# Kernel tuning notes

Measured on AMD Instinct MI355X. Metric: run time of the kernel, lower is better.

## Reference

```python
import jax, jax.numpy as jnp
import numpy as np

N = 50000
D = 128
T = 1024
K = 10
GAMMA = 1.0
CHUNK = 64  # anchors processed per step to avoid a [T,N,D] intermediate


def setup_inputs() -> dict:
    key = jax.random.key(0)
    k1, k2, k3, k4 = jax.random.split(key, 4)
    return {
        "out1": jax.random.normal(k1, (N, D), dtype=jnp.float32),
        "out2": jax.random.normal(k2, (N, D), dtype=jnp.float32),
        "anchor1_org": jax.random.randint(k3, (T,), 0, N, dtype=jnp.int64 if jax.config.jax_enable_x64 else jnp.int32),
        "anchor2_org": jax.random.randint(k4, (T,), 0, N, dtype=jnp.int64 if jax.config.jax_enable_x64 else jnp.int32),
    }


def _mine_neg(anchor_vecs, G):
    # anchor_vecs: [T, D], G: [N, D] -> indices of K nearest (L1) rows of G, [T*K]
    a = anchor_vecs.reshape(T // CHUNK, CHUNK, D)

    def body(chunk):
        # L1 distances [CHUNK, N]
        dist = jnp.sum(jnp.abs(chunk[:, None, :] - G[None, :, :]), axis=-1)
        _, idx = jax.lax.top_k(-dist, K)  # k smallest distances
        return idx

    idx = jax.lax.map(body, a)  # [T//CHUNK, CHUNK, K]
    return idx.reshape(T * K)


def reference(out1, out2, anchor1_org, anchor2_org):
    # negative mining (mirrors cdist + argsort[:k] on detached arrays)
    neg1 = _mine_neg(out1[anchor1_org], out2)  # negatives in graph 2 for anchor1
    neg2 = _mine_neg(out2[anchor2_org], out1)  # negatives in graph 1 for anchor2

    anchor1 = jnp.repeat(anchor1_org, K)  # [T*K]
    anchor2 = jnp.repeat(anchor2_org, K)

    a1 = out1[anchor1]
    a2 = out2[anchor2]
    n1 = out2[neg1]
    n2 = out1[neg2]

    A = jnp.sum(jnp.abs(a1 - a2), axis=1)
    Dm = A + GAMMA
    L1 = jnp.sum(jax.nn.relu(Dm - jnp.sum(jnp.abs(a1 - n1), axis=1)))
    L2 = jnp.sum(jax.nn.relu(Dm - jnp.sum(jnp.abs(a2 - n2), axis=1)))
    return (L1 + L2) / (T * K)
```

## Files before the change

### kernel.cpp

```cpp
#include <hip/hip_runtime.h>
#include <stdint.h>


#define NROWS 50000
#define DDIM  128
#define TT    1024
#define KK    10
#define NCH   64
#define CH    782
#define TILES 16
#define TT2   (2 * TT)
#define TROWS 16

typedef float f32x2 __attribute__((ext_vector_type(2)));
typedef float f32x4 __attribute__((ext_vector_type(4)));

__device__ __forceinline__ void topk_insert(float (&val)[KK], int (&idx)[KK],
                                            float cv, int ci) {
#pragma unroll
  for (int i = 0; i < KK; i++) {
    const bool lt = cv < val[i];
    const float tv = lt ? val[i] : cv;
    const int ti = lt ? idx[i] : ci;
    val[i] = lt ? cv : val[i];
    idx[i] = lt ? ci : idx[i];
    cv = tv;
    ci = ti;
  }
}

__global__ __launch_bounds__(64, 2) void mine_kernel(
    const float* __restrict__ out1, const float* __restrict__ out2,
    const int* __restrict__ anc1, const int* __restrict__ anc2,
    float* __restrict__ cand_val, int* __restrict__ cand_idx) {
  const int lane = threadIdx.x;
  const int bid = blockIdx.x;
  const int chunk = ((bid >> 8) << 3) | (bid & 7);
  const int combo = (bid >> 3) & 31;
  const int dir = combo >> 4;
  const int tile = combo & 15;

  const float* __restrict__ A = dir ? out2 : out1;
  const float* __restrict__ G = dir ? out1 : out2;
  const int* __restrict__ anc = dir ? anc2 : anc1;

  const int a = tile * 64 + lane;
  const int arow = anc[a];

  f32x2 av[DDIM / 2];
  {
    const f32x4* ap = (const f32x4*)(A + (size_t)arow * DDIM);
#pragma unroll
    for (int j = 0; j < DDIM / 4; j++) {
      const f32x4 v = ap[j];
      av[2 * j] = (f32x2){v.x, v.y};
      av[2 * j + 1] = (f32x2){v.z, v.w};
    }
  }

  float val[KK];
  int idx[KK];
#pragma unroll
  for (int i = 0; i < KK; i++) {
    val[i] = 3.4e38f;
    idx[i] = 0;
  }

  const int r0 = chunk * CH;
  const int r1 = (r0 + CH < NROWS) ? (r0 + CH) : NROWS;
  const int nt = (r1 - r0 + TROWS - 1) / TROWS;

  __shared__ float gt[2][TROWS * DDIM];

  auto STAGE = [&](int b, int rs) {
    const float* gsrc = G + (size_t)rs * DDIM + lane * 4;
    float* ldst = &gt[b][0];
#pragma unroll
    for (int c = 0; c < (TROWS * DDIM) / 256; c++) {
      __builtin_amdgcn_global_load_lds(
          (const __attribute__((address_space(1))) uint32_t*)(gsrc + c * 256),
          (__attribute__((address_space(3))) uint32_t*)(ldst + c * 256),
          16, 0, 0);
    }
  };

  auto RS = [&](int ts) { return ts > NROWS - TROWS ? NROWS - TROWS : ts; };

  STAGE(0, RS(r0));
  asm volatile("s_waitcnt vmcnt(0)" ::: "memory");

  int buf = 0;
  for (int t = 0; t < nt; t++) {
    const int ts = r0 + t * TROWS;
    const int rs = RS(ts);
    if (t + 1 < nt) STAGE(buf ^ 1, RS(ts + TROWS));

    const int rend = (ts + TROWS < r1) ? ts + TROWS : r1;
    for (int r = ts; r < rend; r++) {
      const f32x4* lp = (const f32x4*)&gt[buf][(r - rs) * DDIM];
      float c0 = 0.f, c1 = 0.f, c2 = 0.f, c3 = 0.f;
#pragma unroll
      for (int j = 0; j < DDIM / 4; j++) {
        const f32x4 g = lp[j];
        const f32x2 d0 = av[2 * j] - (f32x2){g.x, g.y};
        const f32x2 d1 = av[2 * j + 1] - (f32x2){g.z, g.w};
        c0 += fabsf(d0.x);
        c1 += fabsf(d0.y);
        c2 += fabsf(d1.x);
        c3 += fabsf(d1.y);
      }
      const float acc = (c0 + c1) + (c2 + c3);
      if (acc < val[KK - 1]) topk_insert(val, idx, acc, r);
    }
    asm volatile("s_waitcnt vmcnt(0)" ::: "memory");
    buf ^= 1;
  }

  const int slot = dir * TT + a;
#pragma unroll
  for (int i = 0; i < KK; i++) {
    const size_t o = (size_t)(chunk * KK + i) * TT2 + slot;
    cand_val[o] = val[i];
    cand_idx[o] = idx[i];
  }
}

__global__ void merge_kernel(const float* __restrict__ cand_val,
                             const int* __restrict__ cand_idx,
                             int* __restrict__ neg) {
  const int tid = blockIdx.x * blockDim.x + threadIdx.x;
  if (tid >= TT2) return;
  float val[KK];
  int idx[KK];
#pragma unroll
  for (int i = 0; i < KK; i++) {
    val[i] = 3.4e38f;
    idx[i] = 0;
  }
  for (int c = 0; c < NCH * KK; c++) {
    const float v = cand_val[(size_t)c * TT2 + tid];
    if (v < val[KK - 1]) topk_insert(val, idx, v, cand_idx[(size_t)c * TT2 + tid]);
  }
#pragma unroll
  for (int i = 0; i < KK; i++) neg[(size_t)tid * KK + i] = idx[i];
}

__global__ void zero_kernel(float* __restrict__ out) {
  if (threadIdx.x == 0) out[0] = 0.f;
}

__global__ void loss_kernel(const float* __restrict__ out1,
                            const float* __restrict__ out2,
                            const int* __restrict__ anc1,
                            const int* __restrict__ anc2,
                            const int* __restrict__ neg,
                            float* __restrict__ out) {
  const int lane = threadIdx.x & 63;
  const int w = threadIdx.x >> 6;
  const int t = blockIdx.x * 4 + w;
  const int a1 = anc1[t];
  const int a2 = anc2[t];
  const int e = lane * 2;

  const f32x2 x1 = *(const f32x2*)(out1 + (size_t)a1 * DDIM + e);
  const f32x2 x2 = *(const f32x2*)(out2 + (size_t)a2 * DDIM + e);

  float ap = fabsf(x1.x - x2.x) + fabsf(x1.y - x2.y);
#pragma unroll
  for (int o = 32; o > 0; o >>= 1) ap += __shfl_xor(ap, o, 64);
  const float Dm = ap + 1.0f;

  float s = 0.f;
  for (int k = 0; k < KK; k++) {
    const int n1 = neg[(size_t)t * KK + k];
    const int n2 = neg[(size_t)(TT + t) * KK + k];
    const f32x2 v1 = *(const f32x2*)(out2 + (size_t)n1 * DDIM + e);
    const f32x2 v2 = *(const f32x2*)(out1 + (size_t)n2 * DDIM + e);
    float d1 = fabsf(x1.x - v1.x) + fabsf(x1.y - v1.y);
    float d2 = fabsf(x2.x - v2.x) + fabsf(x2.y - v2.y);
#pragma unroll
    for (int o = 32; o > 0; o >>= 1) {
      d1 += __shfl_xor(d1, o, 64);
      d2 += __shfl_xor(d2, o, 64);
    }
    s += fmaxf(Dm - d1, 0.f) + fmaxf(Dm - d2, 0.f);
  }
  if (lane == 0) atomicAdd(out, s * (1.0f / (TT * KK)));
}

extern "C" void kernel_launch(void* const* d_in, const int* in_sizes, int n_in,
                              void* d_out, int out_size, void* d_ws,
                              size_t ws_size, hipStream_t stream) {
  const float* out1 = (const float*)d_in[0];
  const float* out2 = (const float*)d_in[1];
  const int* anc1 = (const int*)d_in[2];
  const int* anc2 = (const int*)d_in[3];

  float* cand_val = (float*)d_ws;
  int* cand_idx = (int*)(cand_val + (size_t)NCH * KK * TT2);
  int* neg = cand_idx + (size_t)NCH * KK * TT2;
  float* out = (float*)d_out;

  hipLaunchKernelGGL(mine_kernel, dim3(2 * TILES * NCH), dim3(64), 0, stream,
                     out1, out2, anc1, anc2, cand_val, cand_idx);
  hipLaunchKernelGGL(merge_kernel, dim3(8), dim3(256), 0, stream, cand_val,
                     cand_idx, neg);
  hipLaunchKernelGGL(zero_kernel, dim3(1), dim3(64), 0, stream, out);
  hipLaunchKernelGGL(loss_kernel, dim3(TT / 4), dim3(256), 0, stream, out1,
                     out2, anc1, anc2, neg, out);
}
```

Measured before the change: 1.386 ms.

## Split anchor dims across lane pairs, widen mine blocks, two-level top-k merge

Each anchor's 128-dim L1 distance is now split across two lanes that each hold half the vector and combine partial sums with a shuffle. This halves per-thread register use for the anchor and doubles thread parallelism. Mining blocks grow to 256 threads (128 anchors) sharing each staged LDS tile, with __syncthreads replacing per-wave waits. The serial 640-candidate merge is split into a parallel 8-way partial merge followed by a small final merge. The costs are a duplicated top-k insertion in both lanes of each pair and an extra kernel launch.

New measurement: 3.900 ms. +181.4%, slower.

```diff
diff --git a/kernel.cpp b/kernel.cpp
--- a/kernel.cpp
+++ b/kernel.cpp
@@ -8,7 +8,6 @@
 #define KK    10
 #define NCH   64
 #define CH    782
-#define TILES 16
 #define TT2   (2 * TT)
 #define TROWS 16
 
@@ -29,29 +28,32 @@
   }
 }
 
-__global__ __launch_bounds__(64, 2) void mine_kernel(
+__global__ __launch_bounds__(256, 4) void mine_kernel(
     const float* __restrict__ out1, const float* __restrict__ out2,
     const int* __restrict__ anc1, const int* __restrict__ anc2,
     float* __restrict__ cand_val, int* __restrict__ cand_idx) {
-  const int lane = threadIdx.x;
+  const int tid = threadIdx.x;
+  const int lane = tid & 63;
+  const int w = tid >> 6;
   const int bid = blockIdx.x;
-  const int chunk = ((bid >> 8) << 3) | (bid & 7);
-  const int combo = (bid >> 3) & 31;
-  const int dir = combo >> 4;
-  const int tile = combo & 15;
+  const int chunk = ((bid >> 7) << 3) | (bid & 7);
+  const int combo = (bid >> 3) & 15;
+  const int dir = combo >> 3;
+  const int tile = combo & 7;
 
   const float* __restrict__ A = dir ? out2 : out1;
   const float* __restrict__ G = dir ? out1 : out2;
   const int* __restrict__ anc = dir ? anc2 : anc1;
 
-  const int a = tile * 64 + lane;
+  const int half = lane & 1;
+  const int a = tile * 128 + w * 32 + (lane >> 1);
   const int arow = anc[a];
 
-  f32x2 av[DDIM / 2];
+  f32x2 av[DDIM / 4];
   {
-    const f32x4* ap = (const f32x4*)(A + (size_t)arow * DDIM);
-#pragma unroll
-    for (int j = 0; j < DDIM / 4; j++) {
+    const f32x4* ap = (const f32x4*)(A + (size_t)arow * DDIM + half * 64);
+#pragma unroll
+    for (int j = 0; j < 16; j++) {
       const f32x4 v = ap[j];
       av[2 * j] = (f32x2){v.x, v.y};
       av[2 * j + 1] = (f32x2){v.z, v.w};
@@ -73,21 +75,20 @@
   __shared__ float gt[2][TROWS * DDIM];
 
   auto STAGE = [&](int b, int rs) {
-    const float* gsrc = G + (size_t)rs * DDIM + lane * 4;
-    float* ldst = &gt[b][0];
-#pragma unroll
-    for (int c = 0; c < (TROWS * DDIM) / 256; c++) {
+    const float* src = G + (size_t)rs * DDIM + w * 256 + lane * 4;
+    float* dst = &gt[b][w * 256];
+#pragma unroll
+    for (int c = 0; c < 2; c++) {
       __builtin_amdgcn_global_load_lds(
-          (const __attribute__((address_space(1))) uint32_t*)(gsrc + c * 256),
-          (__attribute__((address_space(3))) uint32_t*)(ldst + c * 256),
+          (const __attribute__((address_space(1))) uint32_t*)(src + c * 1024),
+          (__attribute__((address_space(3))) uint32_t*)(dst + c * 1024),
           16, 0, 0);
     }
   };
-
   auto RS = [&](int ts) { return ts > NROWS - TROWS ? NROWS - TROWS : ts; };
 
   STAGE(0, RS(r0));
-  asm volatile("s_waitcnt vmcnt(0)" ::: "memory");
+  __syncthreads();
 
   int buf = 0;
   for (int t = 0; t < nt; t++) {
@@ -97,10 +98,10 @@
 
     const int rend = (ts + TROWS < r1) ? ts + TROWS : r1;
     for (int r = ts; r < rend; r++) {
-      const f32x4* lp = (const f32x4*)&gt[buf][(r - rs) * DDIM];
+      const f32x4* lp = (const f32x4*)&gt[buf][(r - rs) * DDIM + half * 64];
       float c0 = 0.f, c1 = 0.f, c2 = 0.f, c3 = 0.f;
 #pragma unroll
-      for (int j = 0; j < DDIM / 4; j++) {
+      for (int j = 0; j < 16; j++) {
         const f32x4 g = lp[j];
         const f32x2 d0 = av[2 * j] - (f32x2){g.x, g.y};
         const f32x2 d1 = av[2 * j + 1] - (f32x2){g.z, g.w};
@@ -109,27 +110,55 @@
         c2 += fabsf(d1.x);
         c3 += fabsf(d1.y);
       }
-      const float acc = (c0 + c1) + (c2 + c3);
+      const float p = (c0 + c1) + (c2 + c3);
+      const float acc = p + __shfl_xor(p, 1, 64);
       if (acc < val[KK - 1]) topk_insert(val, idx, acc, r);
     }
-    asm volatile("s_waitcnt vmcnt(0)" ::: "memory");
+    __syncthreads();
     buf ^= 1;
   }
 
-  const int slot = dir * TT + a;
-#pragma unroll
-  for (int i = 0; i < KK; i++) {
-    const size_t o = (size_t)(chunk * KK + i) * TT2 + slot;
+  if ((lane & 1) == 0) {
+    const int slot = dir * TT + a;
+#pragma unroll
+    for (int i = 0; i < KK; i++) {
+      const size_t o = (size_t)(chunk * KK + i) * TT2 + slot;
+      cand_val[o] = val[i];
+      cand_idx[o] = idx[i];
+    }
+  }
+}
+
+__global__ void merge1_kernel(float* __restrict__ cand_val,
+                              int* __restrict__ cand_idx) {
+  const int tid = blockIdx.x * blockDim.x + threadIdx.x;
+  const int slot = tid & (TT2 - 1);
+  const int part = tid >> 11;
+  float val[KK];
+  int idx[KK];
+#pragma unroll
+  for (int i = 0; i < KK; i++) {
+    val[i] = 3.4e38f;
+    idx[i] = 0;
+  }
+  for (int q = 0; q < 8 * KK; q++) {
+    const size_t o = (size_t)(part * 8 * KK + q) * TT2 + slot;
+    const float v = cand_val[o];
+    if (v < val[KK - 1]) topk_insert(val, idx, v, cand_idx[o]);
+  }
+#pragma unroll
+  for (int i = 0; i < KK; i++) {
+    const size_t o = (size_t)(part * 8 * KK + i) * TT2 + slot;
     cand_val[o] = val[i];
     cand_idx[o] = idx[i];
   }
 }
 
-__global__ void merge_kernel(const float* __restrict__ cand_val,
-                             const int* __restrict__ cand_idx,
-                             int* __restrict__ neg) {
-  const int tid = blockIdx.x * blockDim.x + threadIdx.x;
-  if (tid >= TT2) return;
+__global__ void merge2_kernel(const float* __restrict__ cand_val,
+                              const int* __restrict__ cand_idx,
+                              int* __restrict__ neg) {
+  const int slot = blockIdx.x * blockDim.x + threadIdx.x;
+  if (slot >= TT2) return;
   float val[KK];
   int idx[KK];
 #pragma unroll
@@ -137,12 +166,14 @@
     val[i] = 3.4e38f;
     idx[i] = 0;
   }
-  for (int c = 0; c < NCH * KK; c++) {
-    const float v = cand_val[(size_t)c * TT2 + tid];
-    if (v < val[KK - 1]) topk_insert(val, idx, v, cand_idx[(size_t)c * TT2 + tid]);
-  }
-#pragma unroll
-  for (int i = 0; i < KK; i++) neg[(size_t)tid * KK + i] = idx[i];
+  for (int part = 0; part < 8; part++)
+    for (int i = 0; i < KK; i++) {
+      const size_t o = (size_t)(part * 8 * KK + i) * TT2 + slot;
+      const float v = cand_val[o];
+      if (v < val[KK - 1]) topk_insert(val, idx, v, cand_idx[o]);
+    }
+#pragma unroll
+  for (int i = 0; i < KK; i++) neg[(size_t)slot * KK + i] = idx[i];
 }
 
 __global__ void zero_kernel(float* __restrict__ out) {
@@ -201,9 +232,11 @@
   int* neg = cand_idx + (size_t)NCH * KK * TT2;
   float* out = (float*)d_out;
 
-  hipLaunchKernelGGL(mine_kernel, dim3(2 * TILES * NCH), dim3(64), 0, stream,
-                     out1, out2, anc1, anc2, cand_val, cand_idx);
-  hipLaunchKernelGGL(merge_kernel, dim3(8), dim3(256), 0, stream, cand_val,
+  hipLaunchKernelGGL(mine_kernel, dim3(1024), dim3(256), 0, stream, out1, out2,
+                     anc1, anc2, cand_val, cand_idx);
+  hipLaunchKernelGGL(merge1_kernel, dim3(64), dim3(256), 0, stream, cand_val,
+                     cand_idx);
+  hipLaunchKernelGGL(merge2_kernel, dim3(8), dim3(256), 0, stream, cand_val,
                      cand_idx, neg);
   hipLaunchKernelGGL(zero_kernel, dim3(1), dim3(64), 0, stream, out);
   hipLaunchKernelGGL(loss_kernel, dim3(TT / 4), dim3(256), 0, stream, out1,
```
